# Kernel optimization log

Measured on AMD Instinct MI355X. Metric: run time of the kernel, lower is better.

## Reference

```python
import jax, jax.numpy as jnp
import numpy as np

N_NODES = 100000
N_EDGES = 1600000
VOCAB = 1000
D_IN = 64
D_H = 128
D_OUT = 1
NEG_SLOPE = 0.2  # PyG GATConv default leaky_relu slope


def setup_inputs() -> dict:
    key = jax.random.key(0)
    ks = jax.random.split(key, 13)
    s_in = 1.0 / np.sqrt(D_IN)
    s_h = 1.0 / np.sqrt(D_H)
    return {
        "x": jax.random.randint(ks[0], (N_NODES,), 0, VOCAB),
        "edge_index": jax.random.randint(ks[1], (2, N_EDGES), 0, N_NODES),
        "node_embeddings": jax.random.normal(ks[2], (VOCAB, D_IN)) * 0.1,
        "W1": jax.random.normal(ks[3], (D_IN, D_H)) * s_in,
        "a_src1": jax.random.normal(ks[4], (D_H,)) * s_h,
        "a_dst1": jax.random.normal(ks[5], (D_H,)) * s_h,
        "b1": jnp.zeros((D_H,)),
        "W2": jax.random.normal(ks[6], (D_H, D_H)) * s_h,
        "a_src2": jax.random.normal(ks[7], (D_H,)) * s_h,
        "a_dst2": jax.random.normal(ks[8], (D_H,)) * s_h,
        "b2": jnp.zeros((D_H,)),
        "W_fc": jax.random.normal(ks[9], (2 * D_H, D_OUT)) * (1.0 / np.sqrt(2 * D_H)),
        "b_fc": jnp.zeros((D_OUT,)),
    }


def segment_softmax(logits, seg, n):
    # numerically-stable softmax over edges grouped by destination node
    mx = jax.ops.segment_max(logits, seg, num_segments=n)
    e = jnp.exp(logits - mx[seg])
    s = jax.ops.segment_sum(e, seg, num_segments=n)
    return e / (s[seg] + 1e-16)


def gat_conv(h, src, dst, W, a_src, a_dst, b):
    # single-head GATConv (PyG defaults: heads=1, negative_slope=0.2, bias)
    h = h @ W                                   # [N, D]
    logit = (h @ a_src)[src] + (h @ a_dst)[dst]  # [E]
    logit = jax.nn.leaky_relu(logit, NEG_SLOPE)
    alpha = segment_softmax(logit, dst, N_NODES)
    out = jax.ops.segment_sum(alpha[:, None] * h[src], dst, num_segments=N_NODES)
    return out + b


def reference(x, edge_index, node_embeddings, W1, a_src1, a_dst1, b1,
              W2, a_src2, a_dst2, b2, W_fc, b_fc):
    h = node_embeddings[x]                      # [N, D_IN]
    src, dst = edge_index[0], edge_index[1]
    # PyG GATConv adds self-loops by default
    loop = jnp.arange(N_NODES)
    src_sl = jnp.concatenate([src, loop])
    dst_sl = jnp.concatenate([dst, loop])
    h = jax.nn.gelu(gat_conv(h, src_sl, dst_sl, W1, a_src1, a_dst1, b1), approximate=False)
    h = jax.nn.gelu(gat_conv(h, src_sl, dst_sl, W2, a_src2, a_dst2, b2), approximate=False)
    # per-edge prediction: concat endpoint features (original edges, no self-loops)
    pair = jnp.concatenate([h[src], h[dst]], axis=-1)   # [E, 2*D_H]
    out = jax.nn.gelu(pair @ W_fc + b_fc, approximate=False)
    return out.squeeze(1)                       # [E]
```

## Files before the change

kernel.cpp:

```cpp
#include <hip/hip_runtime.h>
#include <hip/hip_bf16.h>

#define N_NODES 100000
#define N_EDGES 1600000
#define N_ESL   1700000
#define VOCAB   1000
#define D_IN    64
#define D_H     128
#define NEG_SLOPE 0.2f

#define BSH   7
#define NB    782
#define CAP   3072
#define CHUNK 16384

#define CO_EMB   0
#define CO_W1    64000
#define CO_AS1   72192
#define CO_AD1   72320
#define CO_B1    72448
#define CO_W2    72576
#define CO_AS2   88960
#define CO_AD2   89088
#define CO_B2    89216
#define CO_WFC   89344
#define CO_BFC   89600
#define CO_TOTAL 89601

__device__ __forceinline__ float us2f(unsigned short h){ union{unsigned v; float f;} c; c.v = ((unsigned)h)<<16; return c.f; }
__device__ __forceinline__ float gelu_f(float v){ return 0.5f*v*(1.0f + erff(v*0.7071067811865475f)); }
__device__ __forceinline__ float4 ldf4(const float* p){ return *reinterpret_cast<const float4*>(p); }
__device__ __forceinline__ void stf4(float* p, float4 v){ *reinterpret_cast<float4*>(p) = v; }

__device__ __forceinline__ float wred_sum(float v){
  #pragma unroll
  for (int m=32;m;m>>=1) v += __shfl_xor(v,m,64);
  return v;
}

__global__ __launch_bounds__(64) void k_detect(const unsigned* __restrict__ w, int* __restrict__ flag){
  int t = threadIdx.x;
  float cnt = 0.f;
  #pragma unroll
  for (int i=0;i<2;++i){
    unsigned v = w[t + 64*i];
    unsigned e = (v >> 7) & 0xFFu;
    cnt += (e >= 110u && e <= 126u) ? 1.f : 0.f;
  }
  cnt = wred_sum(cnt);
  if (t==0) *flag = (cnt >= 64.f) ? 1 : 0;
}

__global__ __launch_bounds__(256) void k_setup(const void* p0, const void* p1, const void* p2, const void* p3,
    const void* p4, const void* p5, const void* p6, const void* p7, const void* p8,
    const void* p9, const void* p10, const int* __restrict__ flag, float* __restrict__ c,
    float* __restrict__ va2, float* __restrict__ vd2){
  int b = blockIdx.x;
  if (b == 351){
    int t = threadIdx.x;
    int r = t & 127;
    int f = *flag;
    const float* w2f = (const float*)p5;
    const unsigned short* w2h = (const unsigned short*)p5;
    const float* af = (const float*)((t < 128) ? p6 : p7);
    const unsigned short* ah = (const unsigned short*)((t < 128) ? p6 : p7);
    float s = 0.f;
    for (int j=0;j<D_H;++j){
      float wv = f ? us2f(w2h[r*D_H+j]) : w2f[r*D_H+j];
      float av = f ? us2f(ah[j]) : af[j];
      s = fmaf(wv, av, s);
    }
    if (t < 128) va2[r] = s; else vd2[r] = s;
    return;
  }
  int i = b*256 + threadIdx.x;
  if (i >= CO_TOTAL) return;
  const void* src; int off;
  if      (i < CO_W1 ){ src=p0;  off=i;          }
  else if (i < CO_AS1){ src=p1;  off=i-CO_W1;    }
  else if (i < CO_AD1){ src=p2;  off=i-CO_AS1;   }
  else if (i < CO_B1 ){ src=p3;  off=i-CO_AD1;   }
  else if (i < CO_W2 ){ src=p4;  off=i-CO_B1;    }
  else if (i < CO_AS2){ src=p5;  off=i-CO_W2;    }
  else if (i < CO_AD2){ src=p6;  off=i-CO_AS2;   }
  else if (i < CO_B2 ){ src=p7;  off=i-CO_AD2;   }
  else if (i < CO_WFC){ src=p8;  off=i-CO_B2;    }
  else if (i < CO_BFC){ src=p9;  off=i-CO_WFC;   }
  else               { src=p10; off=i-CO_BFC;   }
  float v = (*flag) ? us2f(((const unsigned short*)src)[off]) : ((const float*)src)[off];
  c[i] = v;
}

__global__ __launch_bounds__(64) void k_table1(const float* __restrict__ cw,
    float* __restrict__ table1, float* __restrict__ as1, float* __restrict__ ad1){
  const float* emb = cw + CO_EMB;
  const float* W1  = cw + CO_W1;
  int v = blockIdx.x; int t = threadIdx.x;
  __shared__ float er[D_IN];
  er[t] = emb[v*D_IN + t];
  __syncthreads();
  int d0 = t, d1 = t + 64;
  float a0 = 0.f, a1 = 0.f;
  for (int k=0;k<D_IN;++k){
    float e = er[k];
    a0 = fmaf(e, W1[k*D_H+d0], a0);
    a1 = fmaf(e, W1[k*D_H+d1], a1);
  }
  table1[v*D_H+d0] = a0; table1[v*D_H+d1] = a1;
  float ps = a0*cw[CO_AS1+d0] + a1*cw[CO_AS1+d1];
  float pd = a0*cw[CO_AD1+d0] + a1*cw[CO_AD1+d1];
  ps = wred_sum(ps); pd = wred_sum(pd);
  if (t==0){ as1[v]=ps; ad1[v]=pd; }
}

__global__ void k_nodelog(const int* __restrict__ x, const float* __restrict__ as1,
    const float* __restrict__ ad1, float* __restrict__ sA1, float* __restrict__ dA1){
  int i = blockIdx.x*blockDim.x + threadIdx.x;
  if (i < N_NODES){ int xs = x[i]; sA1[i] = as1[xs]; dA1[i] = ad1[xs]; }
}

__global__ __launch_bounds__(256) void k_bin(const int* __restrict__ src,
    const int* __restrict__ dst, int* __restrict__ gcur, unsigned* __restrict__ ebuf){
  __shared__ int hist[NB];
  __shared__ int cur[NB];
  int tid = threadIdx.x;
  int base0 = blockIdx.x * CHUNK;
  int n = N_ESL - base0; if (n > CHUNK) n = CHUNK;
  for (int i=tid; i<NB; i+=256) hist[i] = 0;
  __syncthreads();
  for (int k = tid*4; k < n; k += 1024){
    int e = base0 + k;
    int4 d4;
    if (e + 4 <= N_EDGES) d4 = *reinterpret_cast<const int4*>(dst + e);
    else d4 = make_int4(e-N_EDGES, e+1-N_EDGES, e+2-N_EDGES, e+3-N_EDGES);
    atomicAdd(&hist[d4.x>>BSH], 1);
    atomicAdd(&hist[d4.y>>BSH], 1);
    atomicAdd(&hist[d4.z>>BSH], 1);
    atomicAdd(&hist[d4.w>>BSH], 1);
  }
  __syncthreads();
  for (int b=tid; b<NB; b+=256){
    int c = hist[b];
    cur[b] = c ? atomicAdd(&gcur[b], c) : 0;
  }
  __syncthreads();
  for (int k = tid*4; k < n; k += 1024){
    int e = base0 + k;
    int4 d4, s4;
    if (e + 4 <= N_EDGES){
      d4 = *reinterpret_cast<const int4*>(dst + e);
      s4 = *reinterpret_cast<const int4*>(src + e);
    } else {
      d4 = make_int4(e-N_EDGES, e+1-N_EDGES, e+2-N_EDGES, e+3-N_EDGES);
      s4 = d4;
    }
    int p0 = atomicAdd(&cur[d4.x>>BSH], 1);
    if (p0 < CAP) ebuf[(size_t)(d4.x>>BSH)*CAP + p0] = (unsigned)(((d4.x & 127) << 17) | s4.x);
    int p1 = atomicAdd(&cur[d4.y>>BSH], 1);
    if (p1 < CAP) ebuf[(size_t)(d4.y>>BSH)*CAP + p1] = (unsigned)(((d4.y & 127) << 17) | s4.y);
    int p2 = atomicAdd(&cur[d4.z>>BSH], 1);
    if (p2 < CAP) ebuf[(size_t)(d4.z>>BSH)*CAP + p2] = (unsigned)(((d4.z & 127) << 17) | s4.z);
    int p3 = atomicAdd(&cur[d4.w>>BSH], 1);
    if (p3 < CAP) ebuf[(size_t)(d4.w>>BSH)*CAP + p3] = (unsigned)(((d4.w & 127) << 17) | s4.w);
  }
}

__global__ __launch_bounds__(1024) void k_bscan(const int* __restrict__ gcur, int* __restrict__ csrbase){
  int t = threadIdx.x, lane = t & 63, wid = t >> 6;
  int c = (t < NB) ? gcur[t] : 0;
  if (c > CAP) c = CAP;
  int v = c;
  #pragma unroll
  for (int m=1;m<64;m<<=1){ int u = __shfl_up(v,m,64); if (lane>=m) v += u; }
  __shared__ int wsum[16], woff[16];
  if (lane==63) wsum[wid] = v;
  __syncthreads();
  if (t==0){ int run=0; for (int w=0;w<16;++w){ woff[w]=run; run+=wsum[w]; } }
  __syncthreads();
  v += woff[wid];
  if (t < NB) csrbase[t] = v - c;
}

__global__ __launch_bounds__(256) void k_group(const unsigned* __restrict__ ebuf,
    const int* __restrict__ gcur, const int* __restrict__ csrbase,
    int* __restrict__ csr, int* __restrict__ rowoff, int* __restrict__ rowcnt){
  __shared__ unsigned stage[CAP];
  __shared__ int hist[128], cur[128];
  __shared__ int wtot;
  int b = blockIdx.x, tid = threadIdx.x;
  int n = gcur[b]; if (n > CAP) n = CAP;
  int nodeBase = b << BSH;
  int cbase = csrbase[b];
  if (tid < 128) hist[tid] = 0;
  __syncthreads();
  int nv = n & ~3;
  for (int k = tid*4; k < nv; k += 1024){
    uint4 q = *reinterpret_cast<const uint4*>(ebuf + (size_t)b*CAP + k);
    stage[k]   = q.x; atomicAdd(&hist[q.x >> 17], 1);
    stage[k+1] = q.y; atomicAdd(&hist[q.y >> 17], 1);
    stage[k+2] = q.z; atomicAdd(&hist[q.z >> 17], 1);
    stage[k+3] = q.w; atomicAdd(&hist[q.w >> 17], 1);
  }
  for (int k = nv + tid; k < n; k += 256){
    unsigned p = ebuf[(size_t)b*CAP + k];
    stage[k] = p;
    atomicAdd(&hist[p >> 17], 1);
  }
  __syncthreads();
  int v128 = 0;
  if (tid < 128){
    int lane = tid & 63;
    v128 = hist[tid];
    #pragma unroll
    for (int m=1;m<64;m<<=1){ int u = __shfl_up(v128,m,64); if (lane>=m) v128 += u; }
    if (tid == 63) wtot = v128;
  }
  __syncthreads();
  if (tid < 128){
    int incl = v128 + ((tid >= 64) ? wtot : 0);
    int excl = incl - hist[tid];
    int d = nodeBase + tid;
    if (d < N_NODES){ rowoff[d] = cbase + excl; rowcnt[d] = hist[tid]; }
    cur[tid] = excl;
  }
  __syncthreads();
  for (int k=tid; k<n; k+=256){
    unsigned p = stage[k];
    int pos = atomicAdd(&cur[p >> 17], 1);
    csr[cbase + pos] = (int)(p & 0x1FFFFu);
  }
}

template<int MODE>
__global__ __launch_bounds__(256) void k_agg(const int* __restrict__ rowoff,
    const int* __restrict__ rowcnt, const int* __restrict__ csr_src, const int* __restrict__ x,
    const float* __restrict__ sa, const float* __restrict__ danode,
    const float* __restrict__ feat, const float* __restrict__ cw,
    const float* __restrict__ va2, const float* __restrict__ vd2,
    float* __restrict__ out_h, float* __restrict__ p_lo, float* __restrict__ p_hi){
  __shared__ float2 wrb[4][68];
  int lane = threadIdx.x & 63;
  int wid  = threadIdx.x >> 6;
  int node = blockIdx.x*4 + wid;
  if (node >= N_NODES) return;
  int start = rowoff[node];
  int nj = rowcnt[node];
  int end = start + nj;
  float dA = danode[node];

  int c0 = (lane & 31)*4, half = lane >> 5;
  float a0=0.f, a1=0.f, a2=0.f, a3=0.f;

  if (nj <= 64){
    int p = start + lane;
    bool act = p < end;
    int s = 0; float l = -1e30f; int rb_sav = 0;
    if (act){
      s = csr_src[p];
      l = sa[s] + dA; l = (l > 0.f) ? l : NEG_SLOPE*l;
      rb_sav = (MODE == 0 ? x[s] : s) * D_H;
    }
    float mxv = l;
    #pragma unroll
    for (int off=32; off; off>>=1) mxv = fmaxf(mxv, __shfl_xor(mxv, off, 64));
    float e = act ? expf(l - mxv) : 0.f;
    float ssum = e;
    #pragma unroll
    for (int off=32; off; off>>=1) ssum += __shfl_xor(ssum, off, 64);
    float inv = 1.0f/(ssum + 1e-16f);
    wrb[wid][lane] = make_float2(e*inv, __int_as_float(rb_sav));
    if (lane < 4) wrb[wid][64+lane] = make_float2(0.f, 0.f);

    int mid = ((nj >> 1) + 2) & ~3;
    int lo = half ? mid : 0;
    int hi = half ? nj : mid;
    for (int j = lo; j < hi; j += 4){
      float2 q0 = wrb[wid][j],   q1 = wrb[wid][j+1];
      float2 q2 = wrb[wid][j+2], q3 = wrb[wid][j+3];
      float4 f0 = ldf4(feat + __float_as_int(q0.y) + c0);
      float4 f1 = ldf4(feat + __float_as_int(q1.y) + c0);
      float4 f2 = ldf4(feat + __float_as_int(q2.y) + c0);
      float4 f3 = ldf4(feat + __float_as_int(q3.y) + c0);
      a0 = fmaf(q0.x, f0.x, a0); a1 = fmaf(q0.x, f0.y, a1);
      a2 = fmaf(q0.x, f0.z, a2); a3 = fmaf(q0.x, f0.w, a3);
      a0 = fmaf(q1.x, f1.x, a0); a1 = fmaf(q1.x, f1.y, a1);
      a2 = fmaf(q1.x, f1.z, a2); a3 = fmaf(q1.x, f1.w, a3);
      a0 = fmaf(q2.x, f2.x, a0); a1 = fmaf(q2.x, f2.y, a1);
      a2 = fmaf(q2.x, f2.z, a2); a3 = fmaf(q2.x, f2.w, a3);
      a0 = fmaf(q3.x, f3.x, a0); a1 = fmaf(q3.x, f3.y, a1);
      a2 = fmaf(q3.x, f3.z, a2); a3 = fmaf(q3.x, f3.w, a3);
    }
  } else {
    float m = -1e30f, ss = 0.f;
    for (int p = start + lane; p < end; p += 64){
      int s = csr_src[p];
      float l = sa[s] + dA; l = (l > 0.f) ? l : NEG_SLOPE*l;
      float mn = fmaxf(m, l);
      ss = ss*expf(m-mn) + expf(l-mn);
      m = mn;
    }
    #pragma unroll
    for (int off=32; off; off>>=1){
      float mo = __shfl_xor(m, off, 64);
      float so = __shfl_xor(ss, off, 64);
      float mn = fmaxf(m, mo);
      ss = ss*expf(m-mn) + so*expf(mo-mn);
      m = mn;
    }
    float mx = m;
    float inv = 1.0f/(ss + 1e-16f);

    for (int t0 = start; t0 < end; t0 += 64){
      int p = t0 + lane;
      float w = 0.f; int rb = 0;
      if (p < end){
        int s = csr_src[p];
        float l = sa[s] + dA; l = (l > 0.f) ? l : NEG_SLOPE*l;
        w = expf(l - mx)*inv;
        rb = (MODE == 0 ? x[s] : s) * D_H;
      }
      int cnt = end - t0; if (cnt > 64) cnt = 64;
      int mid = (cnt + 1) >> 1;
      int lo = half ? mid : 0;
      int hi = half ? cnt : mid;
      for (int j = lo; j < hi; j += 4){
        int nh = hi - j;
        float w0 = __shfl(w,  j,   64), w1 = __shfl(w,  j+1, 64);
        float w2 = __shfl(w,  j+2, 64), w3 = __shfl(w,  j+3, 64);
        int   r0 = __shfl(rb, j,   64), r1 = __shfl(rb, j+1, 64);
        int   r2 = __shfl(rb, j+2, 64), r3 = __shfl(rb, j+3, 64);
        float4 f0 = make_float4(0.f,0.f,0.f,0.f), f1 = f0, f2 = f0, f3 = f0;
        f0 = ldf4(feat + r0 + c0);
        if (nh > 1) f1 = ldf4(feat + r1 + c0);
        if (nh > 2) f2 = ldf4(feat + r2 + c0);
        if (nh > 3) f3 = ldf4(feat + r3 + c0);
        a0 = fmaf(w0, f0.x, a0); a1 = fmaf(w0, f0.y, a1);
        a2 = fmaf(w0, f0.z, a2); a3 = fmaf(w0, f0.w, a3);
        a0 = fmaf(w1, f1.x, a0); a1 = fmaf(w1, f1.y, a1);
        a2 = fmaf(w1, f1.z, a2); a3 = fmaf(w1, f1.w, a3);
        a0 = fmaf(w2, f2.x, a0); a1 = fmaf(w2, f2.y, a1);
        a2 = fmaf(w2, f2.z, a2); a3 = fmaf(w2, f2.w, a3);
        a0 = fmaf(w3, f3.x, a0); a1 = fmaf(w3, f3.y, a1);
        a2 = fmaf(w3, f3.z, a2); a3 = fmaf(w3, f3.w, a3);
      }
    }
  }

  a0 += __shfl_xor(a0,32,64); a1 += __shfl_xor(a1,32,64);
  a2 += __shfl_xor(a2,32,64); a3 += __shfl_xor(a3,32,64);

  if (MODE == 0){
    float o0 = gelu_f(a0 + cw[CO_B1+c0]);
    float o1 = gelu_f(a1 + cw[CO_B1+c0+1]);
    float o2 = gelu_f(a2 + cw[CO_B1+c0+2]);
    float o3 = gelu_f(a3 + cw[CO_B1+c0+3]);
    if (!half) stf4(out_h + (size_t)node*D_H + c0, make_float4(o0,o1,o2,o3));
    float pl = o0*va2[c0] + o1*va2[c0+1] + o2*va2[c0+2] + o3*va2[c0+3];
    float ph = o0*vd2[c0] + o1*vd2[c0+1] + o2*vd2[c0+2] + o3*vd2[c0+3];
    #pragma unroll
    for (int off=16; off; off>>=1){ pl += __shfl_xor(pl,off,64); ph += __shfl_xor(ph,off,64); }
    if (lane == 0){ p_lo[node] = pl; p_hi[node] = ph; }
  } else if (MODE == 1){
    if (!half) stf4(out_h + (size_t)node*D_H + c0, make_float4(a0,a1,a2,a3));
  } else {
    float o0 = gelu_f(a0 + cw[CO_B2+c0]);
    float o1 = gelu_f(a1 + cw[CO_B2+c0+1]);
    float o2 = gelu_f(a2 + cw[CO_B2+c0+2]);
    float o3 = gelu_f(a3 + cw[CO_B2+c0+3]);
    float pl = o0*cw[CO_WFC+c0]     + o1*cw[CO_WFC+c0+1]
             + o2*cw[CO_WFC+c0+2]   + o3*cw[CO_WFC+c0+3];
    float ph = o0*cw[CO_WFC+D_H+c0]   + o1*cw[CO_WFC+D_H+c0+1]
             + o2*cw[CO_WFC+D_H+c0+2] + o3*cw[CO_WFC+D_H+c0+3];
    #pragma unroll
    for (int off=16; off; off>>=1){ pl += __shfl_xor(pl,off,64); ph += __shfl_xor(ph,off,64); }
    if (lane == 0){ p_lo[node] = pl; p_hi[node] = ph; }
  }
}

__global__ __launch_bounds__(256) void k_post(const float* __restrict__ agg2,
    const float* __restrict__ cw, float* __restrict__ p_lo, float* __restrict__ p_hi){
  __shared__ float xr[64][D_H];
  __shared__ float W[64][D_H];
  const float* W2 = cw + CO_W2;
  int tid = threadIdx.x;
  int cg = tid & 31;
  int rg = tid >> 5;
  int base = blockIdx.x * 64;

  for (int i = tid; i < 64*D_H/4; i += 256){
    int row = i >> 5, c4 = (i & 31) * 4;
    int rr = base + row;
    float4 v = (rr < N_NODES) ? ldf4(agg2 + (size_t)rr*D_H + c4) : make_float4(0.f,0.f,0.f,0.f);
    stf4(&xr[row][c4], v);
  }

  float4 acc[8];
  #pragma unroll
  for (int rs=0; rs<8; ++rs) acc[rs] = make_float4(0.f,0.f,0.f,0.f);

  #pragma unroll
  for (int hk = 0; hk < 2; ++hk){
    __syncthreads();
    for (int i = tid; i < 64*D_H/4; i += 256){
      int k = i >> 5, c4 = (i & 31) * 4;
      stf4(&W[k][c4], ldf4(W2 + (size_t)(hk*64 + k)*D_H + c4));
    }
    __syncthreads();
    for (int k = 0; k < 64; ++k){
      float4 wv = ldf4(&W[k][cg*4]);
      int kk = hk*64 + k;
      #pragma unroll
      for (int rs = 0; rs < 8; ++rs){
        float xv = xr[rs*8 + rg][kk];
        acc[rs].x = fmaf(xv, wv.x, acc[rs].x);
        acc[rs].y = fmaf(xv, wv.y, acc[rs].y);
        acc[rs].z = fmaf(xv, wv.z, acc[rs].z);
        acc[rs].w = fmaf(xv, wv.w, acc[rs].w);
      }
    }
  }

  float4 b2v = ldf4(cw + CO_B2  + cg*4);
  float4 wlo = ldf4(cw + CO_WFC + cg*4);
  float4 whi = ldf4(cw + CO_WFC + D_H + cg*4);
  #pragma unroll
  for (int rs = 0; rs < 8; ++rs){
    int rr = base + rs*8 + rg;
    float o0 = gelu_f(acc[rs].x + b2v.x);
    float o1 = gelu_f(acc[rs].y + b2v.y);
    float o2 = gelu_f(acc[rs].z + b2v.z);
    float o3 = gelu_f(acc[rs].w + b2v.w);
    float pl = o0*wlo.x + o1*wlo.y + o2*wlo.z + o3*wlo.w;
    float ph = o0*whi.x + o1*whi.y + o2*whi.z + o3*whi.w;
    #pragma unroll
    for (int off=16; off; off>>=1){ pl += __shfl_xor(pl,off,64); ph += __shfl_xor(ph,off,64); }
    if (cg == 0 && rr < N_NODES){ p_lo[rr] = pl; p_hi[rr] = ph; }
  }
}

__global__ __launch_bounds__(256) void k_matmul2(float* __restrict__ hbuf, const float* __restrict__ cw){
  const float* W2 = cw + CO_W2;
  __shared__ float xr[16][D_H];
  int tid = threadIdx.x;
  int col = tid & 127, half = tid >> 7;
  int base = blockIdx.x * 64;
  for (int t0=0; t0<64; t0+=16){
    int r0 = base + t0;
    for (int i=tid; i<16*D_H; i+=256){
      int rr = r0 + (i>>7);
      xr[i>>7][i&127] = (rr < N_NODES) ? hbuf[(size_t)rr*D_H + (i&127)] : 0.f;
    }
    __syncthreads();
    float acc[8];
    #pragma unroll
    for (int r=0;r<8;++r) acc[r] = 0.f;
    int rb = half*8;
    for (int k=0;k<D_H;++k){
      float wv = W2[k*D_H + col];
      #pragma unroll
      for (int r=0;r<8;++r) acc[r] = fmaf(xr[rb+r][k], wv, acc[r]);
    }
    #pragma unroll
    for (int r=0;r<8;++r){
      int rr = r0 + rb + r;
      if (rr < N_NODES) hbuf[(size_t)rr*D_H + col] = acc[r];
    }
    __syncthreads();
  }
}

__global__ void k_final(const int* __restrict__ src, const int* __restrict__ dst,
    const float* __restrict__ p_lo, const float* __restrict__ p_hi,
    const float* __restrict__ cw, const int* __restrict__ flag, void* __restrict__ out){
  int q = blockIdx.x*blockDim.x + threadIdx.x;
  int e0 = q*4;
  if (e0 >= N_EDGES) return;
  float bfc = cw[CO_BFC];
  if (e0 + 4 <= N_EDGES){
    int4 s4 = *reinterpret_cast<const int4*>(src + e0);
    int4 d4 = *reinterpret_cast<const int4*>(dst + e0);
    float4 v;
    v.x = gelu_f(p_lo[s4.x] + p_hi[d4.x] + bfc);
    v.y = gelu_f(p_lo[s4.y] + p_hi[d4.y] + bfc);
    v.z = gelu_f(p_lo[s4.z] + p_hi[d4.z] + bfc);
    v.w = gelu_f(p_lo[s4.w] + p_hi[d4.w] + bfc);
    if (*flag){
      __hip_bfloat16* o = (__hip_bfloat16*)out + e0;
      o[0]=__float2bfloat16(v.x); o[1]=__float2bfloat16(v.y);
      o[2]=__float2bfloat16(v.z); o[3]=__float2bfloat16(v.w);
    } else {
      stf4((float*)out + e0, v);
    }
  } else {
    for (int e = e0; e < N_EDGES; ++e){
      float v = gelu_f(p_lo[src[e]] + p_hi[dst[e]] + bfc);
      if (*flag) ((__hip_bfloat16*)out)[e] = __float2bfloat16(v);
      else       ((float*)out)[e] = v;
    }
  }
}

extern "C" void kernel_launch(void* const* d_in, const int* in_sizes, int n_in,
                              void* d_out, int out_size, void* d_ws, size_t ws_size,
                              hipStream_t stream){
  (void)in_sizes; (void)n_in; (void)out_size;
  const int* x  = (const int*)d_in[0];
  const int* ei = (const int*)d_in[1];
  const int* src = ei;
  const int* dst = ei + N_EDGES;

  char* base = (char*)d_ws;
  size_t off = 0;
  auto A = [&](size_t bytes)->size_t{ size_t r = off; off = (off + bytes + 255) & ~(size_t)255; return r; };
  size_t o_flag   = A(4);
  size_t o_cw     = A((size_t)CO_TOTAL*4);
  size_t o_va2    = A(D_H*4);
  size_t o_vd2    = A(D_H*4);
  size_t o_table1 = A((size_t)VOCAB*D_H*4);
  size_t o_as1    = A(VOCAB*4);
  size_t o_ad1    = A(VOCAB*4);
  size_t o_sA1    = A((size_t)N_NODES*4);
  size_t o_dA1    = A((size_t)N_NODES*4);
  size_t o_sA2    = A((size_t)N_NODES*4);
  size_t o_dA2    = A((size_t)N_NODES*4);
  size_t o_rowoff = A((size_t)N_NODES*4);
  size_t o_rowcnt = A((size_t)N_NODES*4);
  size_t o_plo    = A((size_t)N_NODES*4);
  size_t o_phi    = A((size_t)N_NODES*4);
  size_t o_gcur   = A((size_t)NB*4);
  size_t o_cbase  = A((size_t)NB*4);
  size_t o_csr    = A((size_t)N_ESL*4);
  size_t o_big    = A((size_t)N_NODES*D_H*4);
  size_t need_b   = off;
  size_t o_agg2   = A((size_t)N_NODES*D_H*4);
  size_t need_a   = off;

  int*   flag   = (int*)(base + o_flag);
  float* cw     = (float*)(base + o_cw);
  float* va2    = (float*)(base + o_va2);
  float* vd2    = (float*)(base + o_vd2);
  float* table1 = (float*)(base + o_table1);
  float* as1    = (float*)(base + o_as1);
  float* ad1    = (float*)(base + o_ad1);
  float* sA1    = (float*)(base + o_sA1);
  float* dA1    = (float*)(base + o_dA1);
  float* sA2    = (float*)(base + o_sA2);
  float* dA2    = (float*)(base + o_dA2);
  int*   rowoff = (int*)(base + o_rowoff);
  int*   rowcnt = (int*)(base + o_rowcnt);
  float* plo    = (float*)(base + o_plo);
  float* phi    = (float*)(base + o_phi);
  int*   gcur   = (int*)(base + o_gcur);
  int*   cbase  = (int*)(base + o_cbase);
  int*   csr    = (int*)(base + o_csr);
  float* hbuf   = (float*)(base + o_big);
  unsigned* ebuf= (unsigned*)(base + o_big);
  float* agg2   = (float*)(base + o_agg2);

  if (ws_size < need_b) return;
  bool patha = (ws_size >= need_a);

  k_detect<<<1, 64, 0, stream>>>((const unsigned*)d_in[2], flag);
  k_setup<<<352, 256, 0, stream>>>(d_in[2], d_in[3], d_in[4], d_in[5],
      d_in[6], d_in[7], d_in[8], d_in[9], d_in[10], d_in[11], d_in[12], flag, cw, va2, vd2);
  k_table1<<<VOCAB, 64, 0, stream>>>(cw, table1, as1, ad1);
  k_nodelog<<<(N_NODES+255)/256, 256, 0, stream>>>(x, as1, ad1, sA1, dA1);

  hipMemsetAsync(gcur, 0, (size_t)NB*4, stream);
  k_bin<<<(N_ESL+CHUNK-1)/CHUNK, 256, 0, stream>>>(src, dst, gcur, ebuf);
  k_bscan<<<1, 1024, 0, stream>>>(gcur, cbase);
  k_group<<<NB, 256, 0, stream>>>(ebuf, gcur, cbase, csr, rowoff, rowcnt);

  int nagg = (N_NODES+3)/4;
  k_agg<0><<<nagg, 256, 0, stream>>>(rowoff, rowcnt, csr, x, sA1, dA1, table1, cw, va2, vd2, hbuf, sA2, dA2);
  if (patha){
    k_agg<1><<<nagg, 256, 0, stream>>>(rowoff, rowcnt, csr, x, sA2, dA2, hbuf, cw, va2, vd2, agg2, nullptr, nullptr);
    k_post<<<(N_NODES+63)/64, 256, 0, stream>>>(agg2, cw, plo, phi);
  } else {
    k_matmul2<<<(N_NODES+63)/64, 256, 0, stream>>>(hbuf, cw);
    k_agg<2><<<nagg, 256, 0, stream>>>(rowoff, rowcnt, csr, x, sA2, dA2, hbuf, cw, va2, vd2, nullptr, plo, phi);
  }
  k_final<<<(N_EDGES/4+255)/256, 256, 0, stream>>>(src, dst, plo, phi, cw, flag, d_out);
}
```

Before: 363.1 us.

## Assign one node per half-wave in GAT aggregation and pack source logit with row base

The aggregation kernel now maps each 32-lane half-wave to its own destination node (8 nodes per 256-thread block) instead of one wave per node split into halves, which removes the cross-half reduction and the idle lanes on low-degree nodes. The per-source attention logit and feature-row offset are packed into one float2 array, so each edge needs one gather instead of separate logit and x lookups. The memset of the bin counters is folded into the detect kernel to drop one launch. The half-wave mapping lengthens the serial loop for nodes with more than 32 neighbours, and the mode-2 path is still passed the packed buffer cast back to float.

```diff
diff --git a/kernel.cpp b/kernel.cpp
--- a/kernel.cpp
+++ b/kernel.cpp
@@ -38,8 +38,10 @@
   return v;
 }
 
-__global__ __launch_bounds__(64) void k_detect(const unsigned* __restrict__ w, int* __restrict__ flag){
+__global__ __launch_bounds__(64) void k_detect(const unsigned* __restrict__ w, int* __restrict__ flag,
+    int* __restrict__ gcur){
   int t = threadIdx.x;
+  for (int i=t; i<NB; i+=64) gcur[i] = 0;
   float cnt = 0.f;
   #pragma unroll
   for (int i=0;i<2;++i){
@@ -114,9 +116,13 @@
 }
 
 __global__ void k_nodelog(const int* __restrict__ x, const float* __restrict__ as1,
-    const float* __restrict__ ad1, float* __restrict__ sA1, float* __restrict__ dA1){
+    const float* __restrict__ ad1, float2* __restrict__ g1, float* __restrict__ dA1){
   int i = blockIdx.x*blockDim.x + threadIdx.x;
-  if (i < N_NODES){ int xs = x[i]; sA1[i] = as1[xs]; dA1[i] = ad1[xs]; }
+  if (i < N_NODES){
+    int xs = x[i];
+    g1[i] = make_float2(as1[xs], __int_as_float(xs * D_H));
+    dA1[i] = ad1[xs];
+  }
 }
 
 __global__ __launch_bounds__(256) void k_bin(const int* __restrict__ src,
@@ -233,50 +239,49 @@
 
 template<int MODE>
 __global__ __launch_bounds__(256) void k_agg(const int* __restrict__ rowoff,
-    const int* __restrict__ rowcnt, const int* __restrict__ csr_src, const int* __restrict__ x,
-    const float* __restrict__ sa, const float* __restrict__ danode,
+    const int* __restrict__ rowcnt, const int* __restrict__ csr_src,
+    const float2* __restrict__ gpk, const float* __restrict__ danode,
     const float* __restrict__ feat, const float* __restrict__ cw,
     const float* __restrict__ va2, const float* __restrict__ vd2,
     float* __restrict__ out_h, float* __restrict__ p_lo, float* __restrict__ p_hi){
-  __shared__ float2 wrb[4][68];
+  __shared__ float2 wrb[4][2][36];
   int lane = threadIdx.x & 63;
   int wid  = threadIdx.x >> 6;
-  int node = blockIdx.x*4 + wid;
-  if (node >= N_NODES) return;
+  int half = lane >> 5;
+  int hl   = lane & 31;
+  int node = blockIdx.x*8 + wid*2 + half;
   int start = rowoff[node];
   int nj = rowcnt[node];
   int end = start + nj;
   float dA = danode[node];
 
-  int c0 = (lane & 31)*4, half = lane >> 5;
+  int c0 = hl*4;
   float a0=0.f, a1=0.f, a2=0.f, a3=0.f;
 
-  if (nj <= 64){
-    int p = start + lane;
+  if (hl < 4) wrb[wid][half][32+hl] = make_float2(0.f, 0.f);
+
+  if (nj <= 32){
+    int p = start + hl;
     bool act = p < end;
-    int s = 0; float l = -1e30f; int rb_sav = 0;
+    float l = -1e30f; float rbb = 0.f;
     if (act){
-      s = csr_src[p];
-      l = sa[s] + dA; l = (l > 0.f) ? l : NEG_SLOPE*l;
-      rb_sav = (MODE == 0 ? x[s] : s) * D_H;
+      float2 g = gpk[csr_src[p]];
+      l = g.x + dA; l = (l > 0.f) ? l : NEG_SLOPE*l;
+      rbb = g.y;
     }
     float mxv = l;
     #pragma unroll
-    for (int off=32; off; off>>=1) mxv = fmaxf(mxv, __shfl_xor(mxv, off, 64));
+    for (int off=16; off; off>>=1) mxv = fmaxf(mxv, __shfl_xor(mxv, off, 64));
     float e = act ? expf(l - mxv) : 0.f;
     float ssum = e;
     #pragma unroll
-    for (int off=32; off; off>>=1) ssum += __shfl_xor(ssum, off, 64);
+    for (int off=16; off; off>>=1) ssum += __shfl_xor(ssum, off, 64);
     float inv = 1.0f/(ssum + 1e-16f);
-    wrb[wid][lane] = make_float2(e*inv, __int_as_float(rb_sav));
-    if (lane < 4) wrb[wid][64+lane] = make_float2(0.f, 0.f);
-
-    int mid = ((nj >> 1) + 2) & ~3;
-    int lo = half ? mid : 0;
-    int hi = half ? nj : mid;
-    for (int j = lo; j < hi; j += 4){
-      float2 q0 = wrb[wid][j],   q1 = wrb[wid][j+1];
-      float2 q2 = wrb[wid][j+2], q3 = wrb[wid][j+3];
+    wrb[wid][half][hl] = make_float2(e*inv, rbb);
+
+    for (int j = 0; j < nj; j += 4){
+      float2 q0 = wrb[wid][half][j],   q1 = wrb[wid][half][j+1];
+      float2 q2 = wrb[wid][half][j+2], q3 = wrb[wid][half][j+3];
       float4 f0 = ldf4(feat + __float_as_int(q0.y) + c0);
       float4 f1 = ldf4(feat + __float_as_int(q1.y) + c0);
       float4 f2 = ldf4(feat + __float_as_int(q2.y) + c0);
@@ -292,15 +297,15 @@
     }
   } else {
     float m = -1e30f, ss = 0.f;
-    for (int p = start + lane; p < end; p += 64){
-      int s = csr_src[p];
-      float l = sa[s] + dA; l = (l > 0.f) ? l : NEG_SLOPE*l;
+    for (int p = start + hl; p < end; p += 32){
+      float2 g = gpk[csr_src[p]];
+      float l = g.x + dA; l = (l > 0.f) ? l : NEG_SLOPE*l;
       float mn = fmaxf(m, l);
       ss = ss*expf(m-mn) + expf(l-mn);
       m = mn;
     }
     #pragma unroll
-    for (int off=32; off; off>>=1){
+    for (int off=16; off; off>>=1){
       float mo = __shfl_xor(m, off, 64);
       float so = __shfl_xor(ss, off, 64);
       float mn = fmaxf(m, mo);
@@ -310,58 +315,52 @@
     float mx = m;
     float inv = 1.0f/(ss + 1e-16f);
 
-    for (int t0 = start; t0 < end; t0 += 64){
-      int p = t0 + lane;
-      float w = 0.f; int rb = 0;
+    for (int t0 = start; t0 < end; t0 += 32){
+      int p = t0 + hl;
+      float w = 0.f, rbb = 0.f;
       if (p < end){
-        int s = csr_src[p];
-        float l = sa[s] + dA; l = (l > 0.f) ? l : NEG_SLOPE*l;
+        float2 g = gpk[csr_src[p]];
+        float l = g.x + dA; l = (l > 0.f) ? l : NEG_SLOPE*l;
         w = expf(l - mx)*inv;
-        rb = (MODE == 0 ? x[s] : s) * D_H;
+        rbb = g.y;
       }
-      int cnt = end - t0; if (cnt > 64) cnt = 64;
-      int mid = (cnt + 1) >> 1;
-      int lo = half ? mid : 0;
-      int hi = half ? cnt : mid;
-      for (int j = lo; j < hi; j += 4){
-        int nh = hi - j;
-        float w0 = __shfl(w,  j,   64), w1 = __shfl(w,  j+1, 64);
-        float w2 = __shfl(w,  j+2, 64), w3 = __shfl(w,  j+3, 64);
-        int   r0 = __shfl(rb, j,   64), r1 = __shfl(rb, j+1, 64);
-        int   r2 = __shfl(rb, j+2, 64), r3 = __shfl(rb, j+3, 64);
-        float4 f0 = make_float4(0.f,0.f,0.f,0.f), f1 = f0, f2 = f0, f3 = f0;
-        f0 = ldf4(feat + r0 + c0);
-        if (nh > 1) f1 = ldf4(feat + r1 + c0);
-        if (nh > 2) f2 = ldf4(feat + r2 + c0);
-        if (nh > 3) f3 = ldf4(feat + r3 + c0);
-        a0 = fmaf(w0, f0.x, a0); a1 = fmaf(w0, f0.y, a1);
-        a2 = fmaf(w0, f0.z, a2); a3 = fmaf(w0, f0.w, a3);
-        a0 = fmaf(w1, f1.x, a0); a1 = fmaf(w1, f1.y, a1);
-        a2 = fmaf(w1, f1.z, a2); a3 = fmaf(w1, f1.w, a3);
-        a0 = fmaf(w2, f2.x, a0); a1 = fmaf(w2, f2.y, a1);
-        a2 = fmaf(w2, f2.z, a2); a3 = fmaf(w2, f2.w, a3);
-        a0 = fmaf(w3, f3.x, a0); a1 = fmaf(w3, f3.y, a1);
-        a2 = fmaf(w3, f3.z, a2); a3 = fmaf(w3, f3.w, a3);
+      wrb[wid][half][hl] = make_float2(w, rbb);
+      int cn = end - t0; if (cn > 32) cn = 32;
+      for (int j = 0; j < cn; j += 4){
+        float2 q0 = wrb[wid][half][j],   q1 = wrb[wid][half][j+1];
+        float2 q2 = wrb[wid][half][j+2], q3 = wrb[wid][half][j+3];
+        float4 f0 = ldf4(feat + __float_as_int(q0.y) + c0);
+        float4 f1 = ldf4(feat + __float_as_int(q1.y) + c0);
+        float4 f2 = ldf4(feat + __float_as_int(q2.y) + c0);
+        float4 f3 = ldf4(feat + __float_as_int(q3.y) + c0);
+        a0 = fmaf(q0.x, f0.x, a0); a1 = fmaf(q0.x, f0.y, a1);
+        a2 = fmaf(q0.x, f0.z, a2); a3 = fmaf(q0.x, f0.w, a3);
+        a0 = fmaf(q1.x, f1.x, a0); a1 = fmaf(q1.x, f1.y, a1);
+        a2 = fmaf(q1.x, f1.z, a2); a3 = fmaf(q1.x, f1.w, a3);
+        a0 = fmaf(q2.x, f2.x, a0); a1 = fmaf(q2.x, f2.y, a1);
+        a2 = fmaf(q2.x, f2.z, a2); a3 = fmaf(q2.x, f2.w, a3);
+        a0 = fmaf(q3.x, f3.x, a0); a1 = fmaf(q3.x, f3.y, a1);
+        a2 = fmaf(q3.x, f3.z, a2); a3 = fmaf(q3.x, f3.w, a3);
       }
     }
   }
-
-  a0 += __shfl_xor(a0,32,64); a1 += __shfl_xor(a1,32,64);
-  a2 += __shfl_xor(a2,32,64); a3 += __shfl_xor(a3,32,64);
 
   if (MODE == 0){
     float o0 = gelu_f(a0 + cw[CO_B1+c0]);
     float o1 = gelu_f(a1 + cw[CO_B1+c0+1]);
     float o2 = gelu_f(a2 + cw[CO_B1+c0+2]);
     float o3 = gelu_f(a3 + cw[CO_B1+c0+3]);
-    if (!half) stf4(out_h + (size_t)node*D_H + c0, make_float4(o0,o1,o2,o3));
+    stf4(out_h + (size_t)node*D_H + c0, make_float4(o0,o1,o2,o3));
     float pl = o0*va2[c0] + o1*va2[c0+1] + o2*va2[c0+2] + o3*va2[c0+3];
     float ph = o0*vd2[c0] + o1*vd2[c0+1] + o2*vd2[c0+2] + o3*vd2[c0+3];
     #pragma unroll
     for (int off=16; off; off>>=1){ pl += __shfl_xor(pl,off,64); ph += __shfl_xor(ph,off,64); }
-    if (lane == 0){ p_lo[node] = pl; p_hi[node] = ph; }
+    if (hl == 0){
+      ((float2*)p_lo)[node] = make_float2(pl, __int_as_float(node*D_H));
+      p_hi[node] = ph;
+    }
   } else if (MODE == 1){
-    if (!half) stf4(out_h + (size_t)node*D_H + c0, make_float4(a0,a1,a2,a3));
+    stf4(out_h + (size_t)node*D_H + c0, make_float4(a0,a1,a2,a3));
   } else {
     float o0 = gelu_f(a0 + cw[CO_B2+c0]);
     float o1 = gelu_f(a1 + cw[CO_B2+c0+1]);
@@ -373,7 +372,7 @@
              + o2*cw[CO_WFC+D_H+c0+2] + o3*cw[CO_WFC+D_H+c0+3];
     #pragma unroll
     for (int off=16; off; off>>=1){ pl += __shfl_xor(pl,off,64); ph += __shfl_xor(ph,off,64); }
-    if (lane == 0){ p_lo[node] = pl; p_hi[node] = ph; }
+    if (hl == 0){ p_lo[node] = pl; p_hi[node] = ph; }
   }
 }
 
@@ -519,9 +518,9 @@
   size_t o_table1 = A((size_t)VOCAB*D_H*4);
   size_t o_as1    = A(VOCAB*4);
   size_t o_ad1    = A(VOCAB*4);
-  size_t o_sA1    = A((size_t)N_NODES*4);
+  size_t o_g1     = A((size_t)N_NODES*8);
   size_t o_dA1    = A((size_t)N_NODES*4);
-  size_t o_sA2    = A((size_t)N_NODES*4);
+  size_t o_g2     = A((size_t)N_NODES*8);
   size_t o_dA2    = A((size_t)N_NODES*4);
   size_t o_rowoff = A((size_t)N_NODES*4);
   size_t o_rowcnt = A((size_t)N_NODES*4);
@@ -535,50 +534,49 @@
   size_t o_agg2   = A((size_t)N_NODES*D_H*4);
   size_t need_a   = off;
 
-  int*   flag   = (int*)(base + o_flag);
-  float* cw     = (float*)(base + o_cw);
-  float* va2    = (float*)(base + o_va2);
-  float* vd2    = (float*)(base + o_vd2);
-  float* table1 = (float*)(base + o_table1);
-  float* as1    = (float*)(base + o_as1);
-  float* ad1    = (float*)(base + o_ad1);
-  float* sA1    = (float*)(base + o_sA1);
-  float* dA1    = (float*)(base + o_dA1);
-  float* sA2    = (float*)(base + o_sA2);
-  float* dA2    = (float*)(base + o_dA2);
-  int*   rowoff = (int*)(base + o_rowoff);
-  int*   rowcnt = (int*)(base + o_rowcnt);
-  float* plo    = (float*)(base + o_plo);
-  float* phi    = (float*)(base + o_phi);
-  int*   gcur   = (int*)(base + o_gcur);
-  int*   cbase  = (int*)(base + o_cbase);
-  int*   csr    = (int*)(base + o_csr);
-  float* hbuf   = (float*)(base + o_big);
-  unsigned* ebuf= (unsigned*)(base + o_big);
-  float* agg2   = (float*)(base + o_agg2);
+  int*    flag   = (int*)(base + o_flag);
+  float*  cw     = (float*)(base + o_cw);
+  float*  va2    = (float*)(base + o_va2);
+  float*  vd2    = (float*)(base + o_vd2);
+  float*  table1 = (float*)(base + o_table1);
+  float*  as1    = (float*)(base + o_as1);
+  float*  ad1    = (float*)(base + o_ad1);
+  float2* g1     = (float2*)(base + o_g1);
+  float*  dA1    = (float*)(base + o_dA1);
+  float2* g2     = (float2*)(base + o_g2);
+  float*  dA2    = (float*)(base + o_dA2);
+  int*    rowoff = (int*)(base + o_rowoff);
+  int*    rowcnt = (int*)(base + o_rowcnt);
+  float*  plo    = (float*)(base + o_plo);
+  float*  phi    = (float*)(base + o_phi);
+  int*    gcur   = (int*)(base + o_gcur);
+  int*    cbase  = (int*)(base + o_cbase);
+  int*    csr    = (int*)(base + o_csr);
+  float*  hbuf   = (float*)(base + o_big);
+  unsigned* ebuf = (unsigned*)(base + o_big);
+  float*  agg2   = (float*)(base + o_agg2);
 
   if (ws_size < need_b) return;
   bool patha = (ws_size >= need_a);
 
-  k_detect<<<1, 64, 0, stream>>>((const unsigned*)d_in[2], flag);
+  k_detect<<<1, 64, 0, stream>>>((const unsigned*)d_in[2], flag, gcur);
   k_setup<<<352, 256, 0, stream>>>(d_in[2], d_in[3], d_in[4], d_in[5],
       d_in[6], d_in[7], d_in[8], d_in[9], d_in[10], d_in[11], d_in[12], flag, cw, va2, vd2);
   k_table1<<<VOCAB, 64, 0, stream>>>(cw, table1, as1, ad1);
-  k_nodelog<<<(N_NODES+255)/256, 256, 0, stream>>>(x, as1, ad1, sA1, dA1);
-
-  hipMemsetAsync(gcur, 0, (size_t)NB*4, stream);
+  k_nodelog<<<(N_NODES+255)/256, 256, 0, stream>>>(x, as1, ad1, g1, dA1);
+
   k_bin<<<(N_ESL+CHUNK-1)/CHUNK, 256, 0, stream>>>(src, dst, gcur, ebuf);
   k_bscan<<<1, 1024, 0, stream>>>(gcur, cbase);
   k_group<<<NB, 256, 0, stream>>>(ebuf, gcur, cbase, csr, rowoff, rowcnt);
 
-  int nagg = (N_NODES+3)/4;
-  k_agg<0><<<nagg, 256, 0, stream>>>(rowoff, rowcnt, csr, x, sA1, dA1, table1, cw, va2, vd2, hbuf, sA2, dA2);
+  int nagg = N_NODES/8;
+  k_agg<0><<<nagg, 256, 0, stream>>>(rowoff, rowcnt, csr, g1, dA1, table1, cw, va2, vd2, hbuf, (float*)g2, dA2);
   if (patha){
-    k_agg<1><<<nagg, 256, 0, stream>>>(rowoff, rowcnt, csr, x, sA2, dA2, hbuf, cw, va2, vd2, agg2, nullptr, nullptr);
+    k_agg<1><<<nagg, 256, 0, stream>>>(rowoff, rowcnt, csr, g2, dA2, hbuf, cw, va2, vd2, agg2, nullptr, nullptr);
     k_post<<<(N_NODES+63)/64, 256, 0, stream>>>(agg2, cw, plo, phi);
   } else {
     k_matmul2<<<(N_NODES+63)/64, 256, 0, stream>>>(hbuf, cw);
-    k_agg<2><<<nagg, 256, 0, stream>>>(rowoff, rowcnt, csr, x, sA2, dA2, hbuf, cw, va2, vd2, nullptr, plo, phi);
+    k_agg<2><<<nagg, 256, 0, stream>>>(rowoff, rowcnt, csr, g2, dA2, hbuf, cw, va2, vd2, nullptr, plo, phi);
   }
   k_final<<<(N_EDGES/4+255)/256, 256, 0, stream>>>(src, dst, plo, phi, cw, flag, d_out);
 }
```

Measured after the change: 354.1 us. -2.5%, faster.
